# Kernel optimization log

Hardware: AMD Instinct MI355X
Metric: run time of the kernel (lower is better)

The kernel has to match this reference:

```python
import jax, jax.numpy as jnp
import numpy as np

INPUT_DIM = 1024
OUTPUT_DIM = 1000
DEPTH = 10
LAMBDA_REG = 1e-3
N_INTERNAL = 2 ** DEPTH - 1
N_LEAF = 2 ** DEPTH
BATCH = 16384


def setup_inputs() -> dict:
    key = jax.random.key(0)
    k1, k2, k3 = jax.random.split(key, 3)
    X = jax.random.normal(k1, (BATCH, INPUT_DIM), dtype=jnp.float32)
    # torch nn.Linear weight layout: [out_features, in_features]; scaled to keep
    # sigmoid routing probs away from 0/1 saturation (log-reg term).
    W_internal = jax.random.normal(k2, (N_INTERNAL, INPUT_DIM + 1), dtype=jnp.float32) * 0.02
    W_leaf = jax.random.normal(k3, (OUTPUT_DIM, N_LEAF), dtype=jnp.float32) * 0.02
    return {"X": X, "W_internal": W_internal, "W_leaf": W_leaf}


def _tree_paths(X, W_internal):
    B = X.shape[0]
    Xb = jnp.concatenate([jnp.ones((B, 1), X.dtype), X], axis=1)  # [B, D+1]
    logits = jax.nn.sigmoid(Xb @ W_internal.T)                    # [B, N_int]
    routing = jnp.stack([logits, 1.0 - logits], axis=2)           # [B, N_int, 2]
    path = jnp.ones((B, 1), X.dtype)
    reg = jnp.float32(0.0)
    start = 0
    for layer in range(DEPTH):
        n = 2 ** layer
        lp = routing[:, start:start + n, :].reshape(B, 2 * n)     # next_paths [B, 2n]
        path = jnp.repeat(path, 2, axis=1) * lp                   # new path probs [B, 2n]
        # Faithful to source: parent_idx = node_idx // 2 indexes the UPDATED path probs.
        parent = jnp.repeat(path[:, :n], 2, axis=1)               # [B, 2n]
        num = jnp.sum(lp * parent, axis=0)                        # [2n]
        den = jnp.sum(parent, axis=0) + 1e-8                      # [2n]
        alpha = num / den
        factor = LAMBDA_REG * 2.0 ** (-layer)
        reg = reg + factor * jnp.sum(-0.5 * (jnp.log(alpha) + jnp.log(1.0 - alpha)))
        start += n
    return path, reg  # path: [B, 2^DEPTH]


def reference(X, W_internal, W_leaf):
    path_probs, reg = _tree_paths(X, W_internal)
    predictions = path_probs @ W_leaf.T   # [B, output_dim]
    return predictions, reg
```

## Files before the change

### kernel.cpp

```cpp
#include <hip/hip_runtime.h>
#include <hip/hip_bf16.h>

#define B_ROWS 16384
#define K_DIM  1024
#define N_INT  1023
#define N_OUT  1000

using s8vec = __attribute__((ext_vector_type(8))) short;
using f32x4 = __attribute__((ext_vector_type(4))) float;

static const size_t OFF_XB   = 0;
static const size_t OFF_W1   = OFF_XB   + 33554432;
static const size_t OFF_BIAS = OFF_W1   + 2097152;
static const size_t OFF_PROB = OFF_BIAS + 4096;
static const size_t OFF_PATH = OFF_PROB + 33554432;
static const size_t OFF_W2   = OFF_PATH + 33554432;
static const size_t OFF_SG   = OFF_W2   + 2097152;

__device__ __forceinline__ float b2f(ushort u) {
  return __uint_as_float(((unsigned)u) << 16);
}
__device__ __forceinline__ float blo(unsigned u) { return __uint_as_float(u << 16); }
__device__ __forceinline__ float bhi(unsigned u) { return __uint_as_float(u & 0xffff0000u); }
__device__ __forceinline__ ushort f2b(float f) {
  unsigned u = __float_as_uint(f);
  u = u + 0x7FFFu + ((u >> 16) & 1u);
  return (ushort)(u >> 16);
}

__global__ __launch_bounds__(256) void cvt_x(const float4* __restrict__ X,
                                             ushort4* __restrict__ O) {
  const int i = blockIdx.x * 256 + threadIdx.x;
  const float4 v = X[i];
  ushort4 o;
  o.x = f2b(v.x); o.y = f2b(v.y); o.z = f2b(v.z); o.w = f2b(v.w);
  O[i] = o;
}

__global__ __launch_bounds__(256) void cvt_w(const float* __restrict__ Wi,
                                             const float* __restrict__ Wl,
                                             ushort* __restrict__ W1,
                                             ushort* __restrict__ W2,
                                             float* __restrict__ bias) {
  const int idx = blockIdx.x * 256 + threadIdx.x;
  if (idx < (1 << 20)) {
    const int n = idx >> 10, k = idx & 1023;
    const float v = (n < N_INT) ? Wi[n * 1025 + 1 + k] : 0.f;
    W1[idx] = f2b(v);
    if (k == 0) bias[n] = (n < N_INT) ? Wi[n * 1025] : 0.f;
  } else {
    const int j = idx - (1 << 20);
    const int n = j >> 10, k = j & 1023;
    const float v = (n < N_OUT) ? Wl[n * 1024 + k] : 0.f;
    W2[j] = f2b(v);
  }
}

template <int MODE>
__global__ __launch_bounds__(256, 4) void gemm_bt(const ushort* __restrict__ A,
                                                  const ushort* __restrict__ Bm,
                                                  const float* __restrict__ bias,
                                                  void* __restrict__ outp) {
  __shared__ ushort As[2][4096];
  __shared__ ushort Bs[2][4096];
  const int tid = threadIdx.x;
  const int bn = blockIdx.x, bm = blockIdx.y;
  const int lane = tid & 63, wv = tid >> 6;
  const int wm = wv >> 1, wn = wv & 1;
  const int m16 = lane & 15, q = lane >> 4;

  const ushort* a0p = A  + (size_t)(bm * 128 + (tid >> 2)) * 1024 + (tid & 3) * 8;
  const ushort* b0p = Bm + (size_t)(bn * 128 + (tid >> 2)) * 1024 + (tid & 3) * 8;

  f32x4 acc[4][4] = {};

  {
    uint4 ra0 = *(const uint4*)(a0p);
    uint4 ra1 = *(const uint4*)(a0p + 65536);
    uint4 rb0 = *(const uint4*)(b0p);
    uint4 rb1 = *(const uint4*)(b0p + 65536);
    *(uint4*)(As[0] + tid * 8)        = ra0;
    *(uint4*)(As[0] + 2048 + tid * 8) = ra1;
    *(uint4*)(Bs[0] + tid * 8)        = rb0;
    *(uint4*)(Bs[0] + 2048 + tid * 8) = rb1;
  }

  for (int k0 = 0; k0 < 1024; k0 += 32) {
    const int cur = (k0 >> 5) & 1;
    const int nxt = cur ^ 1;
    uint4 ra0, ra1, rb0, rb1;
    const bool more = (k0 + 32) < 1024;
    if (more) {
      ra0 = *(const uint4*)(a0p + k0 + 32);
      ra1 = *(const uint4*)(a0p + 65536 + k0 + 32);
      rb0 = *(const uint4*)(b0p + k0 + 32);
      rb1 = *(const uint4*)(b0p + 65536 + k0 + 32);
    }
    __syncthreads();
    if (more) {
      *(uint4*)(As[nxt] + tid * 8)        = ra0;
      *(uint4*)(As[nxt] + 2048 + tid * 8) = ra1;
      *(uint4*)(Bs[nxt] + tid * 8)        = rb0;
      *(uint4*)(Bs[nxt] + 2048 + tid * 8) = rb1;
    }
    s8vec af[4], bfv[4];
#pragma unroll
    for (int i = 0; i < 4; ++i)
      af[i] = *(const s8vec*)(As[cur] + (wm * 64 + i * 16 + m16) * 32 + q * 8);
#pragma unroll
    for (int j = 0; j < 4; ++j)
      bfv[j] = *(const s8vec*)(Bs[cur] + (wn * 64 + j * 16 + m16) * 32 + q * 8);
#pragma unroll
    for (int i = 0; i < 4; ++i)
#pragma unroll
      for (int j = 0; j < 4; ++j)
        acc[i][j] = __builtin_amdgcn_mfma_f32_16x16x32_bf16(af[i], bfv[j], acc[i][j], 0, 0, 0);
  }

  if (MODE == 0) {
    ushort* P = (ushort*)outp;
#pragma unroll
    for (int i = 0; i < 4; ++i)
#pragma unroll
      for (int r = 0; r < 4; ++r) {
        const int gr = bm * 128 + wm * 64 + i * 16 + q * 4 + r;
#pragma unroll
        for (int j = 0; j < 4; ++j) {
          const int gc = bn * 128 + wn * 64 + j * 16 + m16;
          const float z = acc[i][j][r] + bias[gc];
          const float p = 1.f / (1.f + expf(-z));
          if (gc < N_INT) P[(size_t)gr * 1024 + gc + 1] = f2b(p);
        }
      }
  } else {
    float* O = (float*)outp;
#pragma unroll
    for (int i = 0; i < 4; ++i)
#pragma unroll
      for (int r = 0; r < 4; ++r) {
        const int gr = bm * 128 + wm * 64 + i * 16 + q * 4 + r;
#pragma unroll
        for (int j = 0; j < 4; ++j) {
          const int gc = bn * 128 + wn * 64 + j * 16 + m16;
          if (gc < N_OUT) O[(size_t)gr * 1000 + gc] = acc[i][j][r];
        }
      }
  }
}

__global__ __launch_bounds__(256) void tree_kernel(const ushort* __restrict__ probs,
                                                   ushort* __restrict__ path,
                                                   float* __restrict__ Sg) {
  __shared__ float Ss[4096];
  for (int i = threadIdx.x; i < 4096; i += 256) Ss[i] = 0.f;
  __syncthreads();
  const int lane = threadIdx.x & 63;
  const int gw = blockIdx.x * 4 + (threadIdx.x >> 6);

  float at1[6] = {}, at2[6] = {};
  float ae1[30] = {}, ae2[30] = {};

#pragma unroll 1
  for (int rr = 0; rr < 4; ++rr) {
    const int r = gw * 4 + rr;
    const ushort* prow = probs + (size_t)r * 1024;
    const ushort p6 = prow[64 + lane];
    const uint   p7 = *(const uint*)(prow + 128 + 2 * lane);
    const uint2  p8 = *(const uint2*)(prow + 256 + 4 * lane);
    const uint4  p9 = *(const uint4*)(prow + 512 + 8 * lane);

    float v = 1.f;
#pragma unroll
    for (int t = 1; t <= 6; ++t) {
      const int ell = t - 1;
      const int e = lane >> (6 - t);
      const float p = b2f(prow[(1 << ell) + (e >> 1)]);
      v *= (e & 1) ? (1.f - p) : p;
      if (((lane & ((1 << (6 - t)) - 1)) == 0) && (e < (1 << ell))) {
        const float pj = b2f(prow[(1 << ell) + e]);
        at1[ell] += v;
        at2[ell] += pj * v;
      }
    }

    float w[16];
    {
      const float p = b2f(p6);
      w[1] = v * (1.f - p); w[0] = v * p;
    }
    {
      const int j0 = __shfl((int)p6, 2 * lane);
      const int j1 = __shfl((int)p6, 2 * lane + 1);
      if (lane < 32) {
        ae1[0] += w[0]; ae2[0] += b2f((ushort)j0) * w[0];
        ae1[1] += w[1]; ae2[1] += b2f((ushort)j1) * w[1];
      }
    }
    {
      const float pA = blo(p7), pB = bhi(p7);
      w[3] = w[1] * (1.f - pB); w[2] = w[1] * pB;
      w[1] = w[0] * (1.f - pA); w[0] = w[0] * pA;
    }
    {
      const uint ua = (uint)__shfl((int)p7, 2 * lane);
      const uint ub = (uint)__shfl((int)p7, 2 * lane + 1);
      if (lane < 32) {
        ae1[2] += w[0]; ae2[2] += blo(ua) * w[0];
        ae1[3] += w[1]; ae2[3] += bhi(ua) * w[1];
        ae1[4] += w[2]; ae2[4] += blo(ub) * w[2];
        ae1[5] += w[3]; ae2[5] += bhi(ub) * w[3];
      }
    }
    {
      const float pv[4] = { blo(p8.x), bhi(p8.x), blo(p8.y), bhi(p8.y) };
#pragma unroll
      for (int i = 3; i >= 0; --i) {
        w[2 * i + 1] = w[i] * (1.f - pv[i]);
        w[2 * i]     = w[i] * pv[i];
      }
    }
    {
      const uint u0 = (uint)__shfl((int)p8.x, 2 * lane);
      const uint u1 = (uint)__shfl((int)p8.y, 2 * lane);
      const uint u2 = (uint)__shfl((int)p8.x, 2 * lane + 1);
      const uint u3 = (uint)__shfl((int)p8.y, 2 * lane + 1);
      if (lane < 32) {
        ae1[6]  += w[0]; ae2[6]  += blo(u0) * w[0];
        ae1[7]  += w[1]; ae2[7]  += bhi(u0) * w[1];
        ae1[8]  += w[2]; ae2[8]  += blo(u1) * w[2];
        ae1[9]  += w[3]; ae2[9]  += bhi(u1) * w[3];
        ae1[10] += w[4]; ae2[10] += blo(u2) * w[4];
        ae1[11] += w[5]; ae2[11] += bhi(u2) * w[5];
        ae1[12] += w[6]; ae2[12] += blo(u3) * w[6];
        ae1[13] += w[7]; ae2[13] += bhi(u3) * w[7];
      }
    }
    {
      const uint pv[4] = { p9.x, p9.y, p9.z, p9.w };
#pragma unroll
      for (int i = 7; i >= 0; --i) {
        const float p = (i & 1) ? bhi(pv[i >> 1]) : blo(pv[i >> 1]);
        w[2 * i + 1] = w[i] * (1.f - p);
        w[2 * i]     = w[i] * p;
      }
    }
    {
      uint s_[8];
      s_[0] = (uint)__shfl((int)p9.x, 2 * lane);
      s_[1] = (uint)__shfl((int)p9.y, 2 * lane);
      s_[2] = (uint)__shfl((int)p9.z, 2 * lane);
      s_[3] = (uint)__shfl((int)p9.w, 2 * lane);
      s_[4] = (uint)__shfl((int)p9.x, 2 * lane + 1);
      s_[5] = (uint)__shfl((int)p9.y, 2 * lane + 1);
      s_[6] = (uint)__shfl((int)p9.z, 2 * lane + 1);
      s_[7] = (uint)__shfl((int)p9.w, 2 * lane + 1);
      if (lane < 32) {
#pragma unroll
        for (int i = 0; i < 16; ++i) {
          const uint u = s_[i >> 1];
          const float pj = (i & 1) ? bhi(u) : blo(u);
          ae1[14 + i] += w[i]; ae2[14 + i] += pj * w[i];
        }
      }
    }
    union { ushort u[16]; uint4 q4[2]; } pk;
#pragma unroll
    for (int i = 0; i < 16; ++i) pk.u[i] = f2b(w[i]);
    uint4* dst = (uint4*)(path + (size_t)r * 1024 + lane * 16);
    dst[0] = pk.q4[0];
    dst[1] = pk.q4[1];
  }

#pragma unroll
  for (int t = 1; t <= 6; ++t) {
    const int ell = t - 1;
    const int e = lane >> (6 - t);
    if (((lane & ((1 << (6 - t)) - 1)) == 0) && (e < (1 << ell))) {
      const int node = (1 << ell) - 1 + e;
      atomicAdd(&Ss[node], at1[ell]);
      atomicAdd(&Ss[2048 + node], at2[ell]);
    }
  }
  if (lane < 32) {
#pragma unroll
    for (int ell = 6; ell <= 9; ++ell) {
      const int s = 1 << (ell - 6);
      const int pb = (1 << ell) - 1;
      const int base = 2 * s - 2;
#pragma unroll
      for (int i = 0; i < 2 * s; ++i) {
        const int node = pb + 2 * s * lane + i;
        atomicAdd(&Ss[node], ae1[base + i]);
        atomicAdd(&Ss[2048 + node], ae2[base + i]);
      }
    }
  }
  __syncthreads();
  for (int i = threadIdx.x; i < 1023; i += 256) {
    atomicAdd(&Sg[i], Ss[i]);
    atomicAdd(&Sg[2048 + i], Ss[2048 + i]);
  }
}

__global__ __launch_bounds__(1024) void finalize_kernel(const float* __restrict__ Sg,
                                                        float* __restrict__ outreg) {
  const int tid = threadIdx.x;
  double val = 0.0;
  if (tid < 1023) {
    const int ell = 31 - __clz(tid + 1);
    const double s1 = (double)Sg[tid];
    const double s2 = (double)Sg[2048 + tid];
    const double den = s1 + 1e-8;
    const double a0 = s2 / den;
    const double a1 = (s1 - s2) / den;
    const double f = 1e-3 * (1.0 / (double)(1 << ell));
    val = -0.5 * f * (log(a0) + log(1.0 - a0) + log(a1) + log(1.0 - a1));
  }
#pragma unroll
  for (int o = 32; o > 0; o >>= 1) val += __shfl_down(val, o, 64);
  __shared__ double partd[16];
  if ((tid & 63) == 0) partd[tid >> 6] = val;
  __syncthreads();
  if (tid == 0) {
    double t = 0.0;
    for (int i = 0; i < 16; ++i) t += partd[i];
    outreg[0] = (float)t;
  }
}

extern "C" void kernel_launch(void* const* d_in, const int* in_sizes, int n_in,
                              void* d_out, int out_size, void* d_ws, size_t ws_size,
                              hipStream_t stream) {
  const float* X     = (const float*)d_in[0];
  const float* Wint  = (const float*)d_in[1];
  const float* Wleaf = (const float*)d_in[2];
  float* out = (float*)d_out;
  char* ws = (char*)d_ws;

  ushort* Xb   = (ushort*)(ws + OFF_XB);
  ushort* W1   = (ushort*)(ws + OFF_W1);
  float*  bias = (float*)(ws + OFF_BIAS);
  ushort* prob = (ushort*)(ws + OFF_PROB);
  ushort* path = (ushort*)(ws + OFF_PATH);
  ushort* W2   = (ushort*)(ws + OFF_W2);
  float*  Sg   = (float*)(ws + OFF_SG);

  (void)hipMemsetAsync(ws + OFF_SG, 0, 16384, stream);
  cvt_x<<<16384, 256, 0, stream>>>((const float4*)X, (ushort4*)Xb);
  cvt_w<<<8192, 256, 0, stream>>>(Wint, Wleaf, W1, W2, bias);
  gemm_bt<0><<<dim3(8, 128), 256, 0, stream>>>(Xb, W1, bias, (void*)prob);
  tree_kernel<<<1024, 256, 0, stream>>>(prob, path, Sg);
  gemm_bt<1><<<dim3(8, 128), 256, 0, stream>>>(path, W2, nullptr, (void*)out);
  finalize_kernel<<<1, 1024, 0, stream>>>(Sg, out + (size_t)B_ROWS * N_OUT);
}
```

Baseline: 327.1 us.

## Use direct global-to-LDS loads with swizzle, swap grid order, batch tree loads

The GEMM now loads tiles straight from global memory into LDS with global_load_lds instead of staging them through registers. It drops double buffering for a single buffer plus two barriers per k-step, and XOR-swizzles the LDS layout to avoid bank conflicts. The grid mapping is swapped so consecutive blocks walk M instead of N. The tree kernel prefetches all four rows up front and replaces scattered global reads of the top levels with wave shuffles. Losing the double buffer risks exposing load latency, since the k-loop no longer overlaps loads with MFMA work.

```diff
diff --git a/kernel.cpp b/kernel.cpp
--- a/kernel.cpp
+++ b/kernel.cpp
@@ -26,6 +26,12 @@
   unsigned u = __float_as_uint(f);
   u = u + 0x7FFFu + ((u >> 16) & 1u);
   return (ushort)(u >> 16);
+}
+
+__device__ __forceinline__ void load_lds16(const ushort* g, ushort* l) {
+  __builtin_amdgcn_global_load_lds((const __attribute__((address_space(1))) void*)g,
+                                   (__attribute__((address_space(3))) void*)l,
+                                   16, 0, 0);
 }
 
 __global__ __launch_bounds__(256) void cvt_x(const float4* __restrict__ X,
@@ -61,55 +67,39 @@
                                                   const ushort* __restrict__ Bm,
                                                   const float* __restrict__ bias,
                                                   void* __restrict__ outp) {
-  __shared__ ushort As[2][4096];
-  __shared__ ushort Bs[2][4096];
+  __shared__ ushort As[4096];
+  __shared__ ushort Bs[4096];
   const int tid = threadIdx.x;
-  const int bn = blockIdx.x, bm = blockIdx.y;
+  const int bm = blockIdx.x, bn = blockIdx.y;
   const int lane = tid & 63, wv = tid >> 6;
   const int wm = wv >> 1, wn = wv & 1;
   const int m16 = lane & 15, q = lane >> 4;
-
-  const ushort* a0p = A  + (size_t)(bm * 128 + (tid >> 2)) * 1024 + (tid & 3) * 8;
-  const ushort* b0p = Bm + (size_t)(bn * 128 + (tid >> 2)) * 1024 + (tid & 3) * 8;
+  const int qs = q ^ ((m16 >> 1) & 3);
+
+  const int r0 = tid >> 2;
+  const int qsw = (tid & 3) ^ ((r0 >> 1) & 3);
+  const ushort* aG = A  + (size_t)(bm * 128 + r0) * 1024 + qsw * 8;
+  const ushort* bG = Bm + (size_t)(bn * 128 + r0) * 1024 + qsw * 8;
+  ushort* AsW = As + wv * 512;
+  ushort* BsW = Bs + wv * 512;
 
   f32x4 acc[4][4] = {};
 
-  {
-    uint4 ra0 = *(const uint4*)(a0p);
-    uint4 ra1 = *(const uint4*)(a0p + 65536);
-    uint4 rb0 = *(const uint4*)(b0p);
-    uint4 rb1 = *(const uint4*)(b0p + 65536);
-    *(uint4*)(As[0] + tid * 8)        = ra0;
-    *(uint4*)(As[0] + 2048 + tid * 8) = ra1;
-    *(uint4*)(Bs[0] + tid * 8)        = rb0;
-    *(uint4*)(Bs[0] + 2048 + tid * 8) = rb1;
-  }
-
   for (int k0 = 0; k0 < 1024; k0 += 32) {
-    const int cur = (k0 >> 5) & 1;
-    const int nxt = cur ^ 1;
-    uint4 ra0, ra1, rb0, rb1;
-    const bool more = (k0 + 32) < 1024;
-    if (more) {
-      ra0 = *(const uint4*)(a0p + k0 + 32);
-      ra1 = *(const uint4*)(a0p + 65536 + k0 + 32);
-      rb0 = *(const uint4*)(b0p + k0 + 32);
-      rb1 = *(const uint4*)(b0p + 65536 + k0 + 32);
-    }
+    if (k0) __syncthreads();
+    load_lds16(aG + k0, AsW);
+    load_lds16(aG + 65536 + k0, AsW + 2048);
+    load_lds16(bG + k0, BsW);
+    load_lds16(bG + 65536 + k0, BsW + 2048);
     __syncthreads();
-    if (more) {
-      *(uint4*)(As[nxt] + tid * 8)        = ra0;
-      *(uint4*)(As[nxt] + 2048 + tid * 8) = ra1;
-      *(uint4*)(Bs[nxt] + tid * 8)        = rb0;
-      *(uint4*)(Bs[nxt] + 2048 + tid * 8) = rb1;
-    }
+
     s8vec af[4], bfv[4];
 #pragma unroll
     for (int i = 0; i < 4; ++i)
-      af[i] = *(const s8vec*)(As[cur] + (wm * 64 + i * 16 + m16) * 32 + q * 8);
+      af[i] = *(const s8vec*)(As + (wm * 64 + i * 16 + m16) * 32 + qs * 8);
 #pragma unroll
     for (int j = 0; j < 4; ++j)
-      bfv[j] = *(const s8vec*)(Bs[cur] + (wn * 64 + j * 16 + m16) * 32 + q * 8);
+      bfv[j] = *(const s8vec*)(Bs + (wn * 64 + j * 16 + m16) * 32 + qs * 8);
 #pragma unroll
     for (int i = 0; i < 4; ++i)
 #pragma unroll
@@ -160,24 +150,35 @@
   float at1[6] = {}, at2[6] = {};
   float ae1[30] = {}, ae2[30] = {};
 
-#pragma unroll 1
+  ushort h4[4], p6a[4]; uint p7a[4]; uint2 p8a[4]; uint4 p9a[4];
+#pragma unroll
+  for (int rr = 0; rr < 4; ++rr) {
+    const ushort* prow = probs + (size_t)(gw * 4 + rr) * 1024;
+    h4[rr]  = prow[lane];
+    p6a[rr] = prow[64 + lane];
+    p7a[rr] = *(const uint*)(prow + 128 + 2 * lane);
+    p8a[rr] = *(const uint2*)(prow + 256 + 4 * lane);
+    p9a[rr] = *(const uint4*)(prow + 512 + 8 * lane);
+  }
+
+#pragma unroll
   for (int rr = 0; rr < 4; ++rr) {
     const int r = gw * 4 + rr;
-    const ushort* prow = probs + (size_t)r * 1024;
-    const ushort p6 = prow[64 + lane];
-    const uint   p7 = *(const uint*)(prow + 128 + 2 * lane);
-    const uint2  p8 = *(const uint2*)(prow + 256 + 4 * lane);
-    const uint4  p9 = *(const uint4*)(prow + 512 + 8 * lane);
+    const int hh = (int)h4[rr];
+    const ushort p6 = p6a[rr];
+    const uint   p7 = p7a[rr];
+    const uint2  p8 = p8a[rr];
+    const uint4  p9 = p9a[rr];
 
     float v = 1.f;
 #pragma unroll
     for (int t = 1; t <= 6; ++t) {
       const int ell = t - 1;
       const int e = lane >> (6 - t);
-      const float p = b2f(prow[(1 << ell) + (e >> 1)]);
+      const float p = b2f((ushort)__shfl(hh, (1 << ell) + (e >> 1)));
       v *= (e & 1) ? (1.f - p) : p;
+      const float pj = b2f((ushort)__shfl(hh, ((1 << ell) + e) & 63));
       if (((lane & ((1 << (6 - t)) - 1)) == 0) && (e < (1 << ell))) {
-        const float pj = b2f(prow[(1 << ell) + e]);
         at1[ell] += v;
         at2[ell] += pj * v;
       }
@@ -348,8 +349,8 @@
   (void)hipMemsetAsync(ws + OFF_SG, 0, 16384, stream);
   cvt_x<<<16384, 256, 0, stream>>>((const float4*)X, (ushort4*)Xb);
   cvt_w<<<8192, 256, 0, stream>>>(Wint, Wleaf, W1, W2, bias);
-  gemm_bt<0><<<dim3(8, 128), 256, 0, stream>>>(Xb, W1, bias, (void*)prob);
+  gemm_bt<0><<<dim3(128, 8), 256, 0, stream>>>(Xb, W1, bias, (void*)prob);
   tree_kernel<<<1024, 256, 0, stream>>>(prob, path, Sg);
-  gemm_bt<1><<<dim3(8, 128), 256, 0, stream>>>(path, W2, nullptr, (void*)out);
+  gemm_bt<1><<<dim3(128, 8), 256, 0, stream>>>(path, W2, nullptr, (void*)out);
   finalize_kernel<<<1, 1024, 0, stream>>>(Sg, out + (size_t)B_ROWS * N_OUT);
 }
```

Measured after the change: 306.0 us. 6.5% less time.
